# Performance work log

Measured on AMD Instinct MI355X. Metric: run time of the kernel, lower is better.

The kernel has to match this reference:

```python
import jax, jax.numpy as jnp
import numpy as np

CUTOFF = 5.0
EPS = 1e-8
N_BASIS = 20
N_LAYERS = 3
F = 128
B, A, N = 4, 256, 64
ZMAX = 100


def _linear(x, W, b=None):
    y = jnp.einsum('...i,oi->...o', x, W)
    return y + b if b is not None else y


def _mlp(x, W1, b1, W2, b2):
    return _linear(jax.nn.silu(_linear(x, W1, b1)), W2, b2)


def _poly_cutoff(d):
    # PolynomialCutoff with p = 6
    p = 6.0
    x = d / CUTOFF
    f = (1.0 - ((p + 1.0) * (p + 2.0) / 2.0) * x**6
         + p * (p + 2.0) * x**7
         - (p * (p + 1.0) / 2.0) * x**8)
    return f * (x < 1.0).astype(d.dtype)


def _rbf(d):
    # RadialBesselLayer: sin(n*pi*d/cutoff) / d, n = 1..N_BASIS
    n = jnp.arange(1, N_BASIS + 1, dtype=d.dtype)
    return jnp.sin(n * jnp.pi * d[..., None] / CUTOFF) / (d[..., None] + EPS)


def _gather(feats, neighbors):
    # feats [B,A,...], neighbors [B,A,N] -> [B,A,N,...]
    return jax.vmap(lambda f, idx: f[idx])(feats, neighbors)


def setup_inputs() -> dict:
    key = jax.random.key(0)
    ks = iter(jax.random.split(key, 64))
    s = 0.08  # weight scale
    inp = {
        'atomic_numbers': jax.random.randint(next(ks), (B, A), 0, ZMAX),
        'positions': jax.random.normal(next(ks), (B, A, 3), jnp.float32),
        'neighbors': jax.random.randint(next(ks), (B, A, N), 0, A),
        'neighbor_mask': jnp.ones((B, A, N), jnp.float32),
        'distances': jax.random.uniform(next(ks), (B, A, N), jnp.float32, 0.1, 4.9),
        'distance_vectors': jax.random.normal(next(ks), (B, A, N, 3), jnp.float32),
        'emb': jax.random.normal(next(ks), (ZMAX, F), jnp.float32) * 0.5,
        'me_W': jax.random.normal(next(ks), (N_LAYERS, F, N_BASIS), jnp.float32) * s,
        'me_b': jnp.zeros((N_LAYERS, F), jnp.float32),
        'mn_W1': jax.random.normal(next(ks), (N_LAYERS, F, F), jnp.float32) * s,
        'mn_b1': jnp.zeros((N_LAYERS, F), jnp.float32),
        'mn_W2': jax.random.normal(next(ks), (N_LAYERS, F, F), jnp.float32) * s,
        'mn_b2': jnp.zeros((N_LAYERS, F), jnp.float32),
        'eqc_W': jax.random.normal(next(ks), (N_LAYERS, 1, F), jnp.float32) * s,
        'eqf_W1': jax.random.normal(next(ks), (N_LAYERS, F, F), jnp.float32) * s,
        'eqf_b1': jnp.zeros((N_LAYERS, F), jnp.float32),
        'eqf_W2': jax.random.normal(next(ks), (N_LAYERS, F, F), jnp.float32) * s,
        'eqf_b2': jnp.zeros((N_LAYERS, F), jnp.float32),
        'esu_W1': jax.random.normal(next(ks), (N_LAYERS, F, F), jnp.float32) * s,
        'esu_b1': jnp.zeros((N_LAYERS, F), jnp.float32),
        'esu_W2': jax.random.normal(next(ks), (N_LAYERS, F, F), jnp.float32) * s,
        'esu_b2': jnp.zeros((N_LAYERS, F), jnp.float32),
        'eme_W1': jax.random.normal(next(ks), (N_LAYERS, F, F), jnp.float32) * s,
        'eme_W2': jax.random.normal(next(ks), (N_LAYERS, F, F), jnp.float32) * s,
        'isu_W1': jax.random.normal(next(ks), (N_LAYERS, F, F), jnp.float32) * s,
        'isu_b1': jnp.zeros((N_LAYERS, F), jnp.float32),
        'isu_W2': jax.random.normal(next(ks), (N_LAYERS, F, F), jnp.float32) * s,
        'isu_b2': jnp.zeros((N_LAYERS, F), jnp.float32),
    }
    return inp


def _forward(atomic_numbers, neighbors, neighbor_mask, distances, distance_vectors,
             emb, me_W, me_b, mn_W1, mn_b1, mn_W2, mn_b2, eqc_W,
             eqf_W1, eqf_b1, eqf_W2, eqf_b2, esu_W1, esu_b1, esu_W2, esu_b2,
             eme_W1, eme_W2, isu_W1, isu_b1, isu_W2, isu_b2):
    # ---- EmbeddingNet ----
    inv_node = emb[atomic_numbers]                      # [B,A,F]
    b, a, f = inv_node.shape
    eq_F = jnp.zeros((b, a, 3), inv_node.dtype)         # [B,A,3]
    eq_f = jnp.zeros((b, a, 3, f), inv_node.dtype)      # [B,A,3,F]
    eq_dr = jnp.zeros((b, a, 3, f), inv_node.dtype)     # [B,A,3,F]
    unit = distance_vectors / (distances[..., None] + EPS)  # [B,A,N,3]
    inv_edge = _rbf(distances)                          # [B,A,N,n_basis]
    cutoff = _poly_cutoff(distances)[..., None]         # [B,A,N,1]
    mask = neighbor_mask[..., None]                     # [B,A,N,1]
    mask2 = neighbor_mask[..., None, None]              # [B,A,N,1,1]

    # ---- InteractionNet x N_LAYERS ----
    for l in range(N_LAYERS):
        msg_edge = _linear(inv_edge, me_W[l], me_b[l]) * cutoff           # [B,A,N,F]
        msg_node = _mlp(inv_node, mn_W1[l], mn_b1[l], mn_W2[l], mn_b2[l])  # [B,A,F]
        msg_node_i = msg_node[:, :, None, :]                               # [B,A,1,F]
        msg_node_f = _gather(msg_node, neighbors)                          # [B,A,N,F]
        inv_msg = msg_edge * msg_node_i * msg_node_f                       # [B,A,N,F]
        # double_update_node = False -> no early invariant update
        eq_msg_F = _linear(inv_msg, eqc_W[l]) * unit                       # [B,A,N,3]
        eq_upd_F = (eq_msg_F * mask).sum(axis=2)                           # [B,A,3]
        eq_F = eq_F + eq_upd_F
        eq_msg_feat = _mlp(inv_msg, eqf_W1[l], eqf_b1[l], eqf_W2[l], eqf_b2[l])
        eq_msg_f = eq_msg_feat[..., None, :] * eq_msg_F[..., None]         # [B,A,N,3,F]
        eq_upd_f = (eq_msg_f * mask2).sum(axis=2)                          # [B,A,3,F]
        eq_f = eq_f + eq_upd_f
        dr_edge = _linear(jax.nn.silu(_linear(inv_msg, eme_W1[l])), eme_W2[l])[..., None, :]  # [B,A,N,1,F]
        dr_node_f = _gather(eq_dr, neighbors)                              # [B,A,N,3,F]
        eq_upd_dr = (dr_edge * dr_node_f * mask2).sum(axis=2)              # [B,A,3,F]
        eq_dr = eq_dr + eq_upd_dr
        eq_dr = eq_dr + _mlp(inv_node, esu_W1[l], esu_b1[l], esu_W2[l], esu_b2[l])[:, :, None, :] * eq_upd_f
        inv_upd = -_mlp(inv_node, isu_W1[l], isu_b1[l], isu_W2[l], isu_b2[l]) * jnp.sum(eq_f * eq_dr, axis=-2)
        inv_node = inv_node + inv_upd
    return inv_node, eq_F, eq_f, eq_dr


def reference(atomic_numbers, positions, neighbors, neighbor_mask, distances, distance_vectors,
              emb, me_W, me_b, mn_W1, mn_b1, mn_W2, mn_b2, eqc_W,
              eqf_W1, eqf_b1, eqf_W2, eqf_b2, esu_W1, esu_b1, esu_W2, esu_b2,
              eme_W1, eme_W2, isu_W1, isu_b1, isu_W2, isu_b2):
    # positions unused (requires_dr = False in EmbeddingNet)
    return _forward(atomic_numbers, neighbors, neighbor_mask, distances, distance_vectors,
                    emb, me_W, me_b, mn_W1, mn_b1, mn_W2, mn_b2, eqc_W,
                    eqf_W1, eqf_b1, eqf_W2, eqf_b2, esu_W1, esu_b1, esu_W2, esu_b2,
                    eme_W1, eme_W2, isu_W1, isu_b1, isu_W2, isu_b2)
```

## Files before the change

### kernel.cpp

```cpp
#include <hip/hip_runtime.h>
#include <cstdint>
#include <cstddef>

#define BB   4
#define AA   256
#define NNB  64
#define FF   128
#define NBAS 20
#define NLAY 3
#define BA   (BB*AA)
#define EDG  (BA*NNB)

typedef __attribute__((ext_vector_type(8))) short bf16x8;
typedef __attribute__((ext_vector_type(4))) float f32x4;

__device__ __forceinline__ float silu_f(float x){ return x / (1.0f + __expf(-x)); }

__device__ __forceinline__ unsigned short f2bf(float x){
  unsigned int u = __float_as_uint(x);
  u += 0x7FFFu + ((u >> 16) & 1u);
  return (unsigned short)(u >> 16);
}
__device__ __forceinline__ unsigned int pk2(float a, float b){
  return (unsigned int)f2bf(a) | ((unsigned int)f2bf(b) << 16);
}

__global__ void k_cvtw(const float* __restrict__ a, const float* __restrict__ b,
                       const float* __restrict__ c, const float* __restrict__ d,
                       const float* __restrict__ me,
                       const float* __restrict__ mnW1, const float* __restrict__ mnW2,
                       const float* __restrict__ esW1, const float* __restrict__ esW2,
                       const float* __restrict__ isW1, const float* __restrict__ isW2,
                       unsigned short* __restrict__ out){
  int id = blockIdx.x*256 + threadIdx.x;
  if (id < 196608){
    int reg = id / 49152, off = id - reg*49152;
    const float* src = (reg==0)?a:(reg==1)?b:(reg==2)?c:d;
    out[id] = f2bf(src[off]);
  } else if (id < 208896){
    int p = id - 196608;
    int l = p >> 12;
    int rem = p & 4095;
    int row = rem >> 5, k = rem & 31;
    float v = (k < NBAS) ? me[((size_t)l*FF + row)*NBAS + k] : 0.0f;
    out[id] = f2bf(v);
  } else if (id < 503808){
    int p = id - 208896;
    int mat = p / 49152, rem = p - mat*49152;
    const float* src = (mat==0)?mnW1:(mat==1)?mnW2:(mat==2)?esW1:(mat==3)?esW2:(mat==4)?isW1:isW2;
    out[id] = f2bf(src[rem]);
  }
}

__global__ __launch_bounds__(256) void k_node_mfma(
    const float* __restrict__ X, const int* __restrict__ z,
    const float* __restrict__ emb, float* __restrict__ inv_node,
    const unsigned short* W1a, const float* b1a, const unsigned short* W2a, const float* b2a, float* Ya,
    const unsigned short* W1b, const float* b1b, const unsigned short* W2b, const float* b2b, float* Yb,
    const unsigned short* W1c, const float* b1c, const unsigned short* W2c, const float* b2c, float* Yc,
    int do_emb){
  const unsigned short *W1,*W2; const float *b1,*b2; float* Y;
  if (blockIdx.y==0){ W1=W1a;b1=b1a;W2=W2a;b2=b2a;Y=Ya; }
  else if (blockIdx.y==1){ W1=W1b;b1=b1b;W2=W2b;b2=b2b;Y=Yb; }
  else { W1=W1c;b1=b1c;W2=W2c;b2=b2c;Y=Yc; }
  __shared__ unsigned short Ws[128*136];
  __shared__ unsigned short Xs[64*136];
  const int t = threadIdx.x, w = t>>6, l = t&63;
  const int g = l&15, kg = (l>>4)<<3, r0 = (l>>4)<<2;
  const int gr0 = blockIdx.x*64;
  const int le = w*16 + g;

  {
    int row = t>>2, c0 = (t&3)*32;
    const float* src = do_emb ? (emb + (size_t)z[gr0+row]*FF + c0)
                              : (X   + (size_t)(gr0+row)*FF + c0);
    #pragma unroll
    for (int j=0;j<8;++j){
      float4 v = *(const float4*)(src + j*4);
      if (do_emb && blockIdx.y==0)
        *(float4*)(inv_node + (size_t)(gr0+row)*FF + c0 + j*4) = v;
      uint2 u; u.x = pk2(v.x,v.y); u.y = pk2(v.z,v.w);
      *(uint2*)(&Xs[row*136 + c0 + j*4]) = u;
    }
  }
  #pragma unroll
  for (int c=t; c<2048; c+=256){
    int row = c >> 4, ko = (c & 15) << 3;
    *(int4*)(&Ws[row*136 + ko]) = *(const int4*)(W1 + row*FF + ko);
  }
  __syncthreads();
  bf16x8 xf[4];
  #pragma unroll
  for (int ks=0;ks<4;++ks) xf[ks] = *(const bf16x8*)(&Xs[le*136 + ks*32 + kg]);
  __syncthreads();
  f32x4 acc[8];
  #pragma unroll
  for (int nt=0;nt<8;++nt) acc[nt] = f32x4{0.f,0.f,0.f,0.f};
  #pragma unroll
  for (int nt=0;nt<8;++nt)
    #pragma unroll
    for (int ks=0;ks<4;++ks){
      bf16x8 wfr = *(const bf16x8*)(&Ws[(nt*16+g)*136 + ks*32 + kg]);
      acc[nt] = __builtin_amdgcn_mfma_f32_16x16x32_bf16(wfr, xf[ks], acc[nt], 0,0,0);
    }
  #pragma unroll
  for (int nt=0;nt<8;++nt){
    int o0 = nt*16 + r0;
    float4 bb = *(const float4*)(b1 + o0);
    uint2 u;
    u.x = pk2(silu_f(acc[nt][0]+bb.x), silu_f(acc[nt][1]+bb.y));
    u.y = pk2(silu_f(acc[nt][2]+bb.z), silu_f(acc[nt][3]+bb.w));
    *(uint2*)(&Xs[le*136 + o0]) = u;
  }
  __syncthreads();
  #pragma unroll
  for (int c=t; c<2048; c+=256){
    int row = c >> 4, ko = (c & 15) << 3;
    *(int4*)(&Ws[row*136 + ko]) = *(const int4*)(W2 + row*FF + ko);
  }
  __syncthreads();
  bf16x8 hf[4];
  #pragma unroll
  for (int ks=0;ks<4;++ks) hf[ks] = *(const bf16x8*)(&Xs[le*136 + ks*32 + kg]);
  #pragma unroll
  for (int nt=0;nt<8;++nt) acc[nt] = f32x4{0.f,0.f,0.f,0.f};
  #pragma unroll
  for (int nt=0;nt<8;++nt)
    #pragma unroll
    for (int ks=0;ks<4;++ks){
      bf16x8 wfr = *(const bf16x8*)(&Ws[(nt*16+g)*136 + ks*32 + kg]);
      acc[nt] = __builtin_amdgcn_mfma_f32_16x16x32_bf16(wfr, hf[ks], acc[nt], 0,0,0);
    }
  #pragma unroll
  for (int nt=0;nt<8;++nt){
    int o0 = nt*16 + r0;
    float4 bb = *(const float4*)(b2 + o0);
    float4 o;
    o.x = acc[nt][0]+bb.x; o.y = acc[nt][1]+bb.y;
    o.z = acc[nt][2]+bb.z; o.w = acc[nt][3]+bb.w;
    *(float4*)(Y + (size_t)(gr0 + le)*FF + o0) = o;
  }
}

__global__ __launch_bounds__(256) void k_layer(
    const float* __restrict__ dist, const float* __restrict__ dvec,
    const float* __restrict__ maskp, const int* __restrict__ nbrs,
    const float* __restrict__ msg_node,
    const unsigned short* __restrict__ meWb, const float* __restrict__ meb,
    const float* __restrict__ eqcW,
    const unsigned short* __restrict__ W1eq, const float* __restrict__ b1eq,
    const unsigned short* __restrict__ W1me,
    const unsigned short* __restrict__ W2eq, const float* __restrict__ b2eq,
    const unsigned short* __restrict__ W2me,
    unsigned short* __restrict__ H1, unsigned short* __restrict__ H2,
    const float* __restrict__ eqdrT_prev, float* __restrict__ eqdrT_next,
    const float* __restrict__ esu, const float* __restrict__ isu,
    float* __restrict__ eqF, float* __restrict__ eqf_out,
    float* __restrict__ eqdr, float* __restrict__ inv_node, int first){
  __shared__ unsigned short Xs[128*136];
  __shared__ float scal[128][4];
  __shared__ int   nbq[128];
  __shared__ float eqFred[4][2][3];
  __shared__ float afl1[4][384];
  __shared__ float afl2[4][384];
  __shared__ float prod[2][384];
  const int t = threadIdx.x, w = t>>6, l = t&63;
  const int bid = blockIdx.x, a0 = bid*2;
  const int g = l&15, kg = (l>>4)<<3, r0 = (l>>4)<<2;
  const float c5 = 0.6283185307179586f;

  if (t < 128){
    int e2 = a0*NNB + t;
    int atomt = a0 + (t>>6);
    nbq[t] = (atomt/AA)*AA + nbrs[e2];
  }

  #pragma unroll
  for (int p=0;p<2;++p){
    const int atom = a0 + p;
    const int eg = atom*NNB + w*16 + g;
    const float d = dist[eg];
    const float dinv = 1.0f/(d + 1e-8f);
    const float xx = d*0.2f;
    float x2=xx*xx, x4=x2*x2, x6=x4*x2, x7=x6*xx, x8=x7*xx;
    float ct = 1.0f - 28.0f*x6 + 48.0f*x7 - 21.0f*x8;
    ct = (xx < 1.0f) ? ct : 0.0f;
    bf16x8 rfr;
    #pragma unroll
    for (int i=0;i<8;++i){
      int k = kg + i;
      float v = (k < NBAS) ? __sinf((float)(k+1)*c5*d)*dinv : 0.0f;
      rfr[i] = (short)f2bf(v);
    }
    f32x4 acc[8];
    #pragma unroll
    for (int nt=0;nt<8;++nt){
      bf16x8 wfr = *(const bf16x8*)(meWb + (nt*16 + g)*32 + kg);
      acc[nt] = __builtin_amdgcn_mfma_f32_16x16x32_bf16(wfr, rfr, f32x4{0.f,0.f,0.f,0.f}, 0,0,0);
    }
    const int bbase = (atom/AA)*AA;
    const int nbv = bbase + nbrs[eg];
    float pv = 0.f;
    #pragma unroll
    for (int nt=0;nt<8;++nt){
      int o0 = nt*16 + r0;
      float4 mb = *(const float4*)(meb + o0);
      float4 mi = *(const float4*)(msg_node + (size_t)atom*FF + o0);
      float4 mf = *(const float4*)(msg_node + (size_t)nbv*FF + o0);
      float4 ec = *(const float4*)(eqcW + o0);
      float v0 = (acc[nt][0]+mb.x)*ct*mi.x*mf.x;
      float v1 = (acc[nt][1]+mb.y)*ct*mi.y*mf.y;
      float v2 = (acc[nt][2]+mb.z)*ct*mi.z*mf.z;
      float v3 = (acc[nt][3]+mb.w)*ct*mi.w*mf.w;
      pv = fmaf(v0,ec.x, fmaf(v1,ec.y, fmaf(v2,ec.z, fmaf(v3,ec.w, pv))));
      uint2 u; u.x = pk2(v0,v1); u.y = pk2(v2,v3);
      *(uint2*)(&Xs[(p*64 + w*16 + g)*136 + o0]) = u;
    }
    pv += __shfl_xor(pv,16); pv += __shfl_xor(pv,32);
    float cf0=0.f, cf1=0.f, cf2=0.f;
    if (l < 16){
      float m  = maskp[eg];
      float s0 = pv*dvec[(size_t)eg*3+0]*dinv;
      float s1 = pv*dvec[(size_t)eg*3+1]*dinv;
      float s2 = pv*dvec[(size_t)eg*3+2]*dinv;
      int lr = p*64 + w*16 + g;
      scal[lr][0]=s0; scal[lr][1]=s1; scal[lr][2]=s2; scal[lr][3]=m;
      cf0 = s0*m; cf1 = s1*m; cf2 = s2*m;
    }
    #pragma unroll
    for (int s2=1; s2<16; s2<<=1){
      cf0 += __shfl_xor(cf0,s2); cf1 += __shfl_xor(cf1,s2); cf2 += __shfl_xor(cf2,s2);
    }
    if (l == 0){ eqFred[w][p][0]=cf0; eqFred[w][p][1]=cf1; eqFred[w][p][2]=cf2; }
  }
  __syncthreads();

  bf16x8 xf[2][4];
  #pragma unroll
  for (int ms=0;ms<2;++ms)
    #pragma unroll
    for (int ks=0;ks<4;++ks)
      xf[ms][ks] = *(const bf16x8*)(&Xs[(w*32 + ms*16 + g)*136 + ks*32 + kg]);
  if (t < 6){
    int p = t/3, c = t - p*3;
    float s = eqFred[0][p][c]+eqFred[1][p][c]+eqFred[2][p][c]+eqFred[3][p][c];
    eqF[(a0+p)*3 + c] = first ? s : (eqF[(a0+p)*3 + c] + s);
  }
  __syncthreads();

  #pragma unroll
  for (int c=t; c<2048; c+=256){
    int row = c >> 4, ko = (c & 15) << 3;
    *(int4*)(&Xs[row*136 + ko]) = *(const int4*)(W1eq + row*FF + ko);
  }
  __syncthreads();
  f32x4 acc2[2][8];
  #pragma unroll
  for (int ms=0;ms<2;++ms)
    #pragma unroll
    for (int nt=0;nt<8;++nt) acc2[ms][nt] = f32x4{0.f,0.f,0.f,0.f};
  #pragma unroll
  for (int nt=0;nt<8;++nt)
    #pragma unroll
    for (int ks=0;ks<4;++ks){
      bf16x8 wfr = *(const bf16x8*)(&Xs[(nt*16+g)*136 + ks*32 + kg]);
      #pragma unroll
      for (int ms=0;ms<2;++ms)
        acc2[ms][nt] = __builtin_amdgcn_mfma_f32_16x16x32_bf16(wfr, xf[ms][ks], acc2[ms][nt], 0,0,0);
    }
  #pragma unroll
  for (int ms=0;ms<2;++ms)
    #pragma unroll
    for (int nt=0;nt<8;++nt){
      int o0 = nt*16 + r0;
      float4 bb = *(const float4*)(b1eq + o0);
      uint2 u;
      u.x = pk2(silu_f(acc2[ms][nt][0]+bb.x), silu_f(acc2[ms][nt][1]+bb.y));
      u.y = pk2(silu_f(acc2[ms][nt][2]+bb.z), silu_f(acc2[ms][nt][3]+bb.w));
      *(uint2*)(H1 + (size_t)(bid*128 + w*32 + ms*16 + g)*FF + o0) = u;
    }

  if (!first){
    __syncthreads();
    #pragma unroll
    for (int c=t; c<2048; c+=256){
      int row = c >> 4, ko = (c & 15) << 3;
      *(int4*)(&Xs[row*136 + ko]) = *(const int4*)(W1me + row*FF + ko);
    }
    __syncthreads();
    #pragma unroll
    for (int ms=0;ms<2;++ms)
      #pragma unroll
      for (int nt=0;nt<8;++nt) acc2[ms][nt] = f32x4{0.f,0.f,0.f,0.f};
    #pragma unroll
    for (int nt=0;nt<8;++nt)
      #pragma unroll
      for (int ks=0;ks<4;++ks){
        bf16x8 wfr = *(const bf16x8*)(&Xs[(nt*16+g)*136 + ks*32 + kg]);
        #pragma unroll
        for (int ms=0;ms<2;++ms)
          acc2[ms][nt] = __builtin_amdgcn_mfma_f32_16x16x32_bf16(wfr, xf[ms][ks], acc2[ms][nt], 0,0,0);
      }
    #pragma unroll
    for (int ms=0;ms<2;++ms)
      #pragma unroll
      for (int nt=0;nt<8;++nt){
        int o0 = nt*16 + r0;
        uint2 u;
        u.x = pk2(silu_f(acc2[ms][nt][0]), silu_f(acc2[ms][nt][1]));
        u.y = pk2(silu_f(acc2[ms][nt][2]), silu_f(acc2[ms][nt][3]));
        *(uint2*)(H2 + (size_t)(bid*128 + w*32 + ms*16 + g)*FF + o0) = u;
      }
  }
  __syncthreads();

  bf16x8 hfr1[2][4];
  #pragma unroll
  for (int ms=0;ms<2;++ms)
    #pragma unroll
    for (int ks=0;ks<4;++ks)
      hfr1[ms][ks] = *(const bf16x8*)(H1 + (size_t)(bid*128 + w*32 + ms*16 + g)*FF + ks*32 + kg);
  #pragma unroll
  for (int c=t; c<2048; c+=256){
    int row = c >> 4, ko = (c & 15) << 3;
    *(int4*)(&Xs[row*136 + ko]) = *(const int4*)(W2eq + row*FF + ko);
  }
  __syncthreads();
  f32x4 acc[2][8];
  #pragma unroll
  for (int ms=0;ms<2;++ms)
    #pragma unroll
    for (int nt=0;nt<8;++nt) acc[ms][nt] = f32x4{0.f,0.f,0.f,0.f};
  #pragma unroll
  for (int nt=0;nt<8;++nt)
    #pragma unroll
    for (int ks=0;ks<4;++ks){
      bf16x8 wfr = *(const bf16x8*)(&Xs[(nt*16+g)*136 + ks*32 + kg]);
      #pragma unroll
      for (int ms=0;ms<2;++ms)
        acc[ms][nt] = __builtin_amdgcn_mfma_f32_16x16x32_bf16(hfr1[ms][ks], wfr, acc[ms][nt], 0,0,0);
    }
  #pragma unroll
  for (int nt=0;nt<8;++nt){
    int col = nt*16 + g;
    float bb = b2eq[col];
    float q0=0.f,q1=0.f,q2=0.f;
    #pragma unroll
    for (int ms=0;ms<2;++ms)
      #pragma unroll
      for (int r=0;r<4;++r){
        int row = w*32 + ms*16 + r0 + r;
        float ym = (acc[ms][nt][r] + bb) * scal[row][3];
        q0 = fmaf(ym, scal[row][0], q0);
        q1 = fmaf(ym, scal[row][1], q1);
        q2 = fmaf(ym, scal[row][2], q2);
      }
    q0 += __shfl_xor(q0,16); q0 += __shfl_xor(q0,32);
    q1 += __shfl_xor(q1,16); q1 += __shfl_xor(q1,32);
    q2 += __shfl_xor(q2,16); q2 += __shfl_xor(q2,32);
    if (l < 16){
      afl1[w][0*128+col] = q0; afl1[w][1*128+col] = q1; afl1[w][2*128+col] = q2;
    }
  }
  if (!first){
    bf16x8 hfr2[2][4];
    #pragma unroll
    for (int ms=0;ms<2;++ms)
      #pragma unroll
      for (int ks=0;ks<4;++ks)
        hfr2[ms][ks] = *(const bf16x8*)(H2 + (size_t)(bid*128 + w*32 + ms*16 + g)*FF + ks*32 + kg);
    __syncthreads();
    #pragma unroll
    for (int c=t; c<2048; c+=256){
      int row = c >> 4, ko = (c & 15) << 3;
      *(int4*)(&Xs[row*136 + ko]) = *(const int4*)(W2me + row*FF + ko);
    }
    __syncthreads();
    #pragma unroll
    for (int ms=0;ms<2;++ms)
      #pragma unroll
      for (int nt=0;nt<8;++nt) acc[ms][nt] = f32x4{0.f,0.f,0.f,0.f};
    #pragma unroll
    for (int nt=0;nt<8;++nt)
      #pragma unroll
      for (int ks=0;ks<4;++ks){
        bf16x8 wfr = *(const bf16x8*)(&Xs[(nt*16+g)*136 + ks*32 + kg]);
        #pragma unroll
        for (int ms=0;ms<2;++ms)
          acc[ms][nt] = __builtin_amdgcn_mfma_f32_16x16x32_bf16(hfr2[ms][ks], wfr, acc[ms][nt], 0,0,0);
      }
    #pragma unroll
    for (int nt=0;nt<8;++nt){
      int col = nt*16 + g;
      float q0=0.f,q1=0.f,q2=0.f;
      #pragma unroll
      for (int ms=0;ms<2;++ms)
        #pragma unroll
        for (int r=0;r<4;++r){
          int row = w*32 + ms*16 + r0 + r;
          float ym = acc[ms][nt][r] * scal[row][3];
          float4 gv = *(const float4*)(eqdrT_prev + ((size_t)nbq[row]*FF + col)*4);
          q0 = fmaf(ym, gv.x, q0);
          q1 = fmaf(ym, gv.y, q1);
          q2 = fmaf(ym, gv.z, q2);
        }
      q0 += __shfl_xor(q0,16); q0 += __shfl_xor(q0,32);
      q1 += __shfl_xor(q1,16); q1 += __shfl_xor(q1,32);
      q2 += __shfl_xor(q2,16); q2 += __shfl_xor(q2,32);
      if (l < 16){
        afl2[w][0*128+col] = q0; afl2[w][1*128+col] = q1; afl2[w][2*128+col] = q2;
      }
    }
  }
  __syncthreads();
  for (int i=t; i<768; i+=256){
    int p = (i >= 384) ? 1 : 0;
    int j = i - p*384;
    int o = j & 127;
    int c = j >> 7;
    float s1 = afl1[2*p][j] + afl1[2*p+1][j];
    float s2 = first ? 0.0f : (afl2[2*p][j] + afl2[2*p+1][j]);
    size_t idx = (size_t)(a0+p)*384 + j;
    float ef = first ? s1 : (eqf_out[idx] + s1);
    eqf_out[idx] = ef;
    float es = esu[(size_t)(a0+p)*FF + o];
    float v = (first ? 0.0f : eqdr[idx]) + s2 + es*s1;
    eqdr[idx] = v;
    eqdrT_next[((size_t)(a0+p)*FF + o)*4 + c] = v;
    prod[p][j] = ef * v;
  }
  __syncthreads();
  {
    int p = t >> 7, o = t & 127;
    float sum3 = prod[p][o] + prod[p][128+o] + prod[p][256+o];
    size_t idx = (size_t)(a0+p)*FF + o;
    inv_node[idx] = fmaf(-isu[idx], sum3, inv_node[idx]);
  }
}

extern "C" void kernel_launch(void* const* d_in, const int* in_sizes, int n_in,
                              void* d_out, int out_size, void* d_ws, size_t ws_size,
                              hipStream_t stream){
  const int*   z     = (const int*)  d_in[0];
  const int*   nbrs  = (const int*)  d_in[2];
  const float* maskp = (const float*)d_in[3];
  const float* dist  = (const float*)d_in[4];
  const float* dvec  = (const float*)d_in[5];
  const float* emb   = (const float*)d_in[6];
  const float* me_W  = (const float*)d_in[7];
  const float* me_b  = (const float*)d_in[8];
  const float* mn_W1 = (const float*)d_in[9];
  const float* mn_b1 = (const float*)d_in[10];
  const float* mn_W2 = (const float*)d_in[11];
  const float* mn_b2 = (const float*)d_in[12];
  const float* eqc_W = (const float*)d_in[13];
  const float* eqf_W1= (const float*)d_in[14];
  const float* eqf_b1= (const float*)d_in[15];
  const float* eqf_W2= (const float*)d_in[16];
  const float* eqf_b2= (const float*)d_in[17];
  const float* esu_W1= (const float*)d_in[18];
  const float* esu_b1= (const float*)d_in[19];
  const float* esu_W2= (const float*)d_in[20];
  const float* esu_b2= (const float*)d_in[21];
  const float* eme_W1= (const float*)d_in[22];
  const float* eme_W2= (const float*)d_in[23];
  const float* isu_W1= (const float*)d_in[24];
  const float* isu_b1= (const float*)d_in[25];
  const float* isu_W2= (const float*)d_in[26];
  const float* isu_b2= (const float*)d_in[27];

  float* out      = (float*)d_out;
  float* inv_node = out;
  float* eqF      = out + 131072;
  float* eqf      = out + 134144;
  float* eqdr     = out + 527360;

  float* w        = (float*)d_ws;
  float* msg_node = w;
  float* esu_o    = w + 131072;
  float* isu_o    = w + 262144;
  float* eqdrT_A  = w + 393216;
  float* eqdrT_B  = w + 917504;
  unsigned short* wbf = (unsigned short*)(w + 1441792);
  unsigned short* H1  = (unsigned short*)(w + 1693696);
  unsigned short* H2  = (unsigned short*)(w + 5888000);

  k_cvtw<<<1968, 256, 0, stream>>>(eqf_W1, eqf_W2, eme_W1, eme_W2, me_W,
      mn_W1, mn_W2, esu_W1, esu_W2, isu_W1, isu_W2, wbf);

  const unsigned short* mnW1b0  = wbf + 208896;
  const unsigned short* mnW2b0  = wbf + 258048;
  const unsigned short* esW1b0  = wbf + 307200;
  const unsigned short* esW2b0  = wbf + 356352;
  const unsigned short* isW1b0  = wbf + 405504;
  const unsigned short* isW2b0  = wbf + 454656;

  k_node_mfma<<<dim3(BA/64, 3), 256, 0, stream>>>(nullptr, z, emb, inv_node,
      mnW1b0, mn_b1,  mnW2b0, mn_b2,  msg_node,
      esW1b0, esu_b1, esW2b0, esu_b2, esu_o,
      isW1b0, isu_b1, isW2b0, isu_b2, isu_o, 1);

  for (int l=0; l<NLAY; ++l){
    size_t oB = (size_t)l*FF;
    const unsigned short* eqfW1b = wbf + 0*49152 + l*16384;
    const unsigned short* eqfW2b = wbf + 1*49152 + l*16384;
    const unsigned short* emeW1b = wbf + 2*49152 + l*16384;
    const unsigned short* emeW2b = wbf + 3*49152 + l*16384;
    const unsigned short* meWb   = wbf + 196608  + l*4096;
    float* dT_prev = (l & 1) ? eqdrT_B : eqdrT_A;
    float* dT_next = (l & 1) ? eqdrT_A : eqdrT_B;
    int first = (l==0);

    k_layer<<<BA/2, 256, 0, stream>>>(dist, dvec, maskp, nbrs, msg_node,
        meWb, me_b+oB, eqc_W+oB,
        eqfW1b, eqf_b1+oB, emeW1b,
        eqfW2b, eqf_b2+oB, emeW2b,
        H1, H2, dT_prev, dT_next, esu_o, isu_o,
        eqF, eqf, eqdr, inv_node, first);
    if (l < NLAY-1){
      size_t oBn = (size_t)(l+1)*FF;
      k_node_mfma<<<dim3(BA/64, 3), 256, 0, stream>>>(inv_node, nullptr, nullptr, nullptr,
          mnW1b0 + (l+1)*16384, mn_b1+oBn,  mnW2b0 + (l+1)*16384, mn_b2+oBn,  msg_node,
          esW1b0 + (l+1)*16384, esu_b1+oBn, esW2b0 + (l+1)*16384, esu_b2+oBn, esu_o,
          isW1b0 + (l+1)*16384, isu_b1+oBn, isW2b0 + (l+1)*16384, isu_b2+oBn, isu_o, 0);
    }
  }
}
```

Before: 164.6 us.

## Keep MLP hidden activations in shared memory instead of global scratch

Hidden activations H1/H2 from the two edge MLPs now go to an LDS tile instead of global workspace, and the computation is reordered so each MLP's second GEMM follows its first. The reduction buffers are merged into one reused array, with intermediate eqf values carried in registers. This removes the global write and read-back of large bf16 hidden tensors per layer. The cost is a second 128x136 bf16 LDS tile, which could lower occupancy, plus more barriers.

```diff
diff --git a/kernel.cpp b/kernel.cpp
--- a/kernel.cpp
+++ b/kernel.cpp
@@ -152,18 +152,16 @@
     const unsigned short* __restrict__ W1me,
     const unsigned short* __restrict__ W2eq, const float* __restrict__ b2eq,
     const unsigned short* __restrict__ W2me,
-    unsigned short* __restrict__ H1, unsigned short* __restrict__ H2,
     const float* __restrict__ eqdrT_prev, float* __restrict__ eqdrT_next,
     const float* __restrict__ esu, const float* __restrict__ isu,
     float* __restrict__ eqF, float* __restrict__ eqf_out,
     float* __restrict__ eqdr, float* __restrict__ inv_node, int first){
-  __shared__ unsigned short Xs[128*136];
+  __shared__ unsigned short Ws[128*136];
+  __shared__ unsigned short Hs[128*136];
   __shared__ float scal[128][4];
   __shared__ int   nbq[128];
+  __shared__ float red[4][384];
   __shared__ float eqFred[4][2][3];
-  __shared__ float afl1[4][384];
-  __shared__ float afl2[4][384];
-  __shared__ float prod[2][384];
   const int t = threadIdx.x, w = t>>6, l = t&63;
   const int bid = blockIdx.x, a0 = bid*2;
   const int g = l&15, kg = (l>>4)<<3, r0 = (l>>4)<<2;
@@ -214,7 +212,7 @@
       float v3 = (acc[nt][3]+mb.w)*ct*mi.w*mf.w;
       pv = fmaf(v0,ec.x, fmaf(v1,ec.y, fmaf(v2,ec.z, fmaf(v3,ec.w, pv))));
       uint2 u; u.x = pk2(v0,v1); u.y = pk2(v2,v3);
-      *(uint2*)(&Xs[(p*64 + w*16 + g)*136 + o0]) = u;
+      *(uint2*)(&Ws[(p*64 + w*16 + g)*136 + o0]) = u;
     }
     pv += __shfl_xor(pv,16); pv += __shfl_xor(pv,32);
     float cf0=0.f, cf1=0.f, cf2=0.f;
@@ -240,7 +238,7 @@
   for (int ms=0;ms<2;++ms)
     #pragma unroll
     for (int ks=0;ks<4;++ks)
-      xf[ms][ks] = *(const bf16x8*)(&Xs[(w*32 + ms*16 + g)*136 + ks*32 + kg]);
+      xf[ms][ks] = *(const bf16x8*)(&Ws[(w*32 + ms*16 + g)*136 + ks*32 + kg]);
   if (t < 6){
     int p = t/3, c = t - p*3;
     float s = eqFred[0][p][c]+eqFred[1][p][c]+eqFred[2][p][c]+eqFred[3][p][c];
@@ -251,7 +249,7 @@
   #pragma unroll
   for (int c=t; c<2048; c+=256){
     int row = c >> 4, ko = (c & 15) << 3;
-    *(int4*)(&Xs[row*136 + ko]) = *(const int4*)(W1eq + row*FF + ko);
+    *(int4*)(&Ws[row*136 + ko]) = *(const int4*)(W1eq + row*FF + ko);
   }
   __syncthreads();
   f32x4 acc2[2][8];
@@ -263,7 +261,7 @@
   for (int nt=0;nt<8;++nt)
     #pragma unroll
     for (int ks=0;ks<4;++ks){
-      bf16x8 wfr = *(const bf16x8*)(&Xs[(nt*16+g)*136 + ks*32 + kg]);
+      bf16x8 wfr = *(const bf16x8*)(&Ws[(nt*16+g)*136 + ks*32 + kg]);
       #pragma unroll
       for (int ms=0;ms<2;++ms)
         acc2[ms][nt] = __builtin_amdgcn_mfma_f32_16x16x32_bf16(wfr, xf[ms][ks], acc2[ms][nt], 0,0,0);
@@ -277,15 +275,79 @@
       uint2 u;
       u.x = pk2(silu_f(acc2[ms][nt][0]+bb.x), silu_f(acc2[ms][nt][1]+bb.y));
       u.y = pk2(silu_f(acc2[ms][nt][2]+bb.z), silu_f(acc2[ms][nt][3]+bb.w));
-      *(uint2*)(H1 + (size_t)(bid*128 + w*32 + ms*16 + g)*FF + o0) = u;
-    }
+      *(uint2*)(&Hs[(w*32 + ms*16 + g)*136 + o0]) = u;
+    }
+  __syncthreads();
+  #pragma unroll
+  for (int c=t; c<2048; c+=256){
+    int row = c >> 4, ko = (c & 15) << 3;
+    *(int4*)(&Ws[row*136 + ko]) = *(const int4*)(W2eq + row*FF + ko);
+  }
+  __syncthreads();
+  {
+    bf16x8 hfr[2][4];
+    #pragma unroll
+    for (int ms=0;ms<2;++ms)
+      #pragma unroll
+      for (int ks=0;ks<4;++ks)
+        hfr[ms][ks] = *(const bf16x8*)(&Hs[(w*32 + ms*16 + g)*136 + ks*32 + kg]);
+    #pragma unroll
+    for (int ms=0;ms<2;++ms)
+      #pragma unroll
+      for (int nt=0;nt<8;++nt) acc2[ms][nt] = f32x4{0.f,0.f,0.f,0.f};
+    #pragma unroll
+    for (int nt=0;nt<8;++nt)
+      #pragma unroll
+      for (int ks=0;ks<4;++ks){
+        bf16x8 wfr = *(const bf16x8*)(&Ws[(nt*16+g)*136 + ks*32 + kg]);
+        #pragma unroll
+        for (int ms=0;ms<2;++ms)
+          acc2[ms][nt] = __builtin_amdgcn_mfma_f32_16x16x32_bf16(hfr[ms][ks], wfr, acc2[ms][nt], 0,0,0);
+      }
+    #pragma unroll
+    for (int nt=0;nt<8;++nt){
+      int col = nt*16 + g;
+      float bb = b2eq[col];
+      float q0=0.f,q1=0.f,q2=0.f;
+      #pragma unroll
+      for (int ms=0;ms<2;++ms)
+        #pragma unroll
+        for (int r=0;r<4;++r){
+          int row = w*32 + ms*16 + r0 + r;
+          float ym = (acc2[ms][nt][r] + bb) * scal[row][3];
+          q0 = fmaf(ym, scal[row][0], q0);
+          q1 = fmaf(ym, scal[row][1], q1);
+          q2 = fmaf(ym, scal[row][2], q2);
+        }
+      q0 += __shfl_xor(q0,16); q0 += __shfl_xor(q0,32);
+      q1 += __shfl_xor(q1,16); q1 += __shfl_xor(q1,32);
+      q2 += __shfl_xor(q2,16); q2 += __shfl_xor(q2,32);
+      if (l < 16){
+        red[w][0*128+col] = q0; red[w][1*128+col] = q1; red[w][2*128+col] = q2;
+      }
+    }
+  }
+  __syncthreads();
+
+  float ef_reg[3], s1_reg[3];
+  {
+    int k = 0;
+    for (int i=t; i<768; i+=256, ++k){
+      int p = (i >= 384) ? 1 : 0;
+      int j = i - p*384;
+      float s1 = red[2*p][j] + red[2*p+1][j];
+      size_t idx = (size_t)(a0+p)*384 + j;
+      float ef = first ? s1 : (eqf_out[idx] + s1);
+      eqf_out[idx] = ef;
+      ef_reg[k] = ef; s1_reg[k] = s1;
+    }
+  }
 
   if (!first){
-    __syncthreads();
     #pragma unroll
     for (int c=t; c<2048; c+=256){
       int row = c >> 4, ko = (c & 15) << 3;
-      *(int4*)(&Xs[row*136 + ko]) = *(const int4*)(W1me + row*FF + ko);
+      *(int4*)(&Ws[row*136 + ko]) = *(const int4*)(W1me + row*FF + ko);
     }
     __syncthreads();
     #pragma unroll
@@ -296,7 +358,7 @@
     for (int nt=0;nt<8;++nt)
       #pragma unroll
       for (int ks=0;ks<4;++ks){
-        bf16x8 wfr = *(const bf16x8*)(&Xs[(nt*16+g)*136 + ks*32 + kg]);
+        bf16x8 wfr = *(const bf16x8*)(&Ws[(nt*16+g)*136 + ks*32 + kg]);
         #pragma unroll
         for (int ms=0;ms<2;++ms)
           acc2[ms][nt] = __builtin_amdgcn_mfma_f32_16x16x32_bf16(wfr, xf[ms][ks], acc2[ms][nt], 0,0,0);
@@ -309,85 +371,33 @@
         uint2 u;
         u.x = pk2(silu_f(acc2[ms][nt][0]), silu_f(acc2[ms][nt][1]));
         u.y = pk2(silu_f(acc2[ms][nt][2]), silu_f(acc2[ms][nt][3]));
-        *(uint2*)(H2 + (size_t)(bid*128 + w*32 + ms*16 + g)*FF + o0) = u;
+        *(uint2*)(&Hs[(w*32 + ms*16 + g)*136 + o0]) = u;
       }
-  }
-  __syncthreads();
-
-  bf16x8 hfr1[2][4];
-  #pragma unroll
-  for (int ms=0;ms<2;++ms)
-    #pragma unroll
-    for (int ks=0;ks<4;++ks)
-      hfr1[ms][ks] = *(const bf16x8*)(H1 + (size_t)(bid*128 + w*32 + ms*16 + g)*FF + ks*32 + kg);
-  #pragma unroll
-  for (int c=t; c<2048; c+=256){
-    int row = c >> 4, ko = (c & 15) << 3;
-    *(int4*)(&Xs[row*136 + ko]) = *(const int4*)(W2eq + row*FF + ko);
-  }
-  __syncthreads();
-  f32x4 acc[2][8];
-  #pragma unroll
-  for (int ms=0;ms<2;++ms)
-    #pragma unroll
-    for (int nt=0;nt<8;++nt) acc[ms][nt] = f32x4{0.f,0.f,0.f,0.f};
-  #pragma unroll
-  for (int nt=0;nt<8;++nt)
-    #pragma unroll
-    for (int ks=0;ks<4;++ks){
-      bf16x8 wfr = *(const bf16x8*)(&Xs[(nt*16+g)*136 + ks*32 + kg]);
-      #pragma unroll
-      for (int ms=0;ms<2;++ms)
-        acc[ms][nt] = __builtin_amdgcn_mfma_f32_16x16x32_bf16(hfr1[ms][ks], wfr, acc[ms][nt], 0,0,0);
-    }
-  #pragma unroll
-  for (int nt=0;nt<8;++nt){
-    int col = nt*16 + g;
-    float bb = b2eq[col];
-    float q0=0.f,q1=0.f,q2=0.f;
-    #pragma unroll
-    for (int ms=0;ms<2;++ms)
-      #pragma unroll
-      for (int r=0;r<4;++r){
-        int row = w*32 + ms*16 + r0 + r;
-        float ym = (acc[ms][nt][r] + bb) * scal[row][3];
-        q0 = fmaf(ym, scal[row][0], q0);
-        q1 = fmaf(ym, scal[row][1], q1);
-        q2 = fmaf(ym, scal[row][2], q2);
-      }
-    q0 += __shfl_xor(q0,16); q0 += __shfl_xor(q0,32);
-    q1 += __shfl_xor(q1,16); q1 += __shfl_xor(q1,32);
-    q2 += __shfl_xor(q2,16); q2 += __shfl_xor(q2,32);
-    if (l < 16){
-      afl1[w][0*128+col] = q0; afl1[w][1*128+col] = q1; afl1[w][2*128+col] = q2;
-    }
-  }
-  if (!first){
-    bf16x8 hfr2[2][4];
-    #pragma unroll
-    for (int ms=0;ms<2;++ms)
-      #pragma unroll
-      for (int ks=0;ks<4;++ks)
-        hfr2[ms][ks] = *(const bf16x8*)(H2 + (size_t)(bid*128 + w*32 + ms*16 + g)*FF + ks*32 + kg);
     __syncthreads();
     #pragma unroll
     for (int c=t; c<2048; c+=256){
       int row = c >> 4, ko = (c & 15) << 3;
-      *(int4*)(&Xs[row*136 + ko]) = *(const int4*)(W2me + row*FF + ko);
+      *(int4*)(&Ws[row*136 + ko]) = *(const int4*)(W2me + row*FF + ko);
     }
     __syncthreads();
+    bf16x8 hfr[2][4];
     #pragma unroll
     for (int ms=0;ms<2;++ms)
       #pragma unroll
-      for (int nt=0;nt<8;++nt) acc[ms][nt] = f32x4{0.f,0.f,0.f,0.f};
+      for (int ks=0;ks<4;++ks)
+        hfr[ms][ks] = *(const bf16x8*)(&Hs[(w*32 + ms*16 + g)*136 + ks*32 + kg]);
+    #pragma unroll
+    for (int ms=0;ms<2;++ms)
+      #pragma unroll
+      for (int nt=0;nt<8;++nt) acc2[ms][nt] = f32x4{0.f,0.f,0.f,0.f};
     #pragma unroll
     for (int nt=0;nt<8;++nt)
       #pragma unroll
       for (int ks=0;ks<4;++ks){
-        bf16x8 wfr = *(const bf16x8*)(&Xs[(nt*16+g)*136 + ks*32 + kg]);
+        bf16x8 wfr = *(const bf16x8*)(&Ws[(nt*16+g)*136 + ks*32 + kg]);
         #pragma unroll
         for (int ms=0;ms<2;++ms)
-          acc[ms][nt] = __builtin_amdgcn_mfma_f32_16x16x32_bf16(hfr2[ms][ks], wfr, acc[ms][nt], 0,0,0);
+          acc2[ms][nt] = __builtin_amdgcn_mfma_f32_16x16x32_bf16(hfr[ms][ks], wfr, acc2[ms][nt], 0,0,0);
       }
     #pragma unroll
     for (int nt=0;nt<8;++nt){
@@ -398,7 +408,7 @@
         #pragma unroll
         for (int r=0;r<4;++r){
           int row = w*32 + ms*16 + r0 + r;
-          float ym = acc[ms][nt][r] * scal[row][3];
+          float ym = acc2[ms][nt][r] * scal[row][3];
           float4 gv = *(const float4*)(eqdrT_prev + ((size_t)nbq[row]*FF + col)*4);
           q0 = fmaf(ym, gv.x, q0);
           q1 = fmaf(ym, gv.y, q1);
@@ -408,31 +418,32 @@
       q1 += __shfl_xor(q1,16); q1 += __shfl_xor(q1,32);
       q2 += __shfl_xor(q2,16); q2 += __shfl_xor(q2,32);
       if (l < 16){
-        afl2[w][0*128+col] = q0; afl2[w][1*128+col] = q1; afl2[w][2*128+col] = q2;
+        red[w][0*128+col] = q0; red[w][1*128+col] = q1; red[w][2*128+col] = q2;
       }
     }
-  }
-  __syncthreads();
-  for (int i=t; i<768; i+=256){
-    int p = (i >= 384) ? 1 : 0;
-    int j = i - p*384;
-    int o = j & 127;
-    int c = j >> 7;
-    float s1 = afl1[2*p][j] + afl1[2*p+1][j];
-    float s2 = first ? 0.0f : (afl2[2*p][j] + afl2[2*p+1][j]);
-    size_t idx = (size_t)(a0+p)*384 + j;
-    float ef = first ? s1 : (eqf_out[idx] + s1);
-    eqf_out[idx] = ef;
-    float es = esu[(size_t)(a0+p)*FF + o];
-    float v = (first ? 0.0f : eqdr[idx]) + s2 + es*s1;
-    eqdr[idx] = v;
-    eqdrT_next[((size_t)(a0+p)*FF + o)*4 + c] = v;
-    prod[p][j] = ef * v;
+    __syncthreads();
+  }
+
+  {
+    int k = 0;
+    for (int i=t; i<768; i+=256, ++k){
+      int p = (i >= 384) ? 1 : 0;
+      int j = i - p*384;
+      int o = j & 127;
+      int c = j >> 7;
+      float s2 = first ? 0.0f : (red[2*p][j] + red[2*p+1][j]);
+      size_t idx = (size_t)(a0+p)*384 + j;
+      float es = esu[(size_t)(a0+p)*FF + o];
+      float v = (first ? 0.0f : eqdr[idx]) + s2 + es*s1_reg[k];
+      eqdr[idx] = v;
+      eqdrT_next[((size_t)(a0+p)*FF + o)*4 + c] = v;
+      red[2*p][j] = ef_reg[k] * v;
+    }
   }
   __syncthreads();
   {
     int p = t >> 7, o = t & 127;
-    float sum3 = prod[p][o] + prod[p][128+o] + prod[p][256+o];
+    float sum3 = red[2*p][o] + red[2*p][128+o] + red[2*p][256+o];
     size_t idx = (size_t)(a0+p)*FF + o;
     inv_node[idx] = fmaf(-isu[idx], sum3, inv_node[idx]);
   }
@@ -482,8 +493,6 @@
   float* eqdrT_A  = w + 393216;
   float* eqdrT_B  = w + 917504;
   unsigned short* wbf = (unsigned short*)(w + 1441792);
-  unsigned short* H1  = (unsigned short*)(w + 1693696);
-  unsigned short* H2  = (unsigned short*)(w + 5888000);
 
   k_cvtw<<<1968, 256, 0, stream>>>(eqf_W1, eqf_W2, eme_W1, eme_W2, me_W,
       mn_W1, mn_W2, esu_W1, esu_W2, isu_W1, isu_W2, wbf);
@@ -515,7 +524,7 @@
         meWb, me_b+oB, eqc_W+oB,
         eqfW1b, eqf_b1+oB, emeW1b,
         eqfW2b, eqf_b2+oB, emeW2b,
-        H1, H2, dT_prev, dT_next, esu_o, isu_o,
+        dT_prev, dT_next, esu_o, isu_o,
         eqF, eqf, eqdr, inv_node, first);
     if (l < NLAY-1){
       size_t oBn = (size_t)(l+1)*FF;
```

New measurement: 142.4 us. 1.16x faster.
